# Kernel tuning notes

Measured on AMD Instinct MI355X. Metric: run time of the kernel, lower is better.

## Reference

```python
import jax, jax.numpy as jnp
import numpy as np

SEQ_LEN = 168; PRED_LEN = 24; N_FEAT = 8; KERNEL = 25
N_QUBITS = 4; N_QLAYERS = 2; CONTEXT = 32; HIDDEN = 8; BATCH = 16384
LAG_POSITIONS = [1, 2, 3, 4, 5, 6, 23, 24, 25, 167, 168]
LAG_IDX = np.array([SEQ_LEN - l for l in LAG_POSITIONS if l <= SEQ_LEN])
N_LAGS = int(LAG_IDX.size)
PI = float(np.pi)


def _apply_1q(state, U, w):
    # apply 2x2 gate U (shared (2,2) or per-sample (B,2,2)) on wire w
    state = jnp.moveaxis(state, 1 + w, -1)
    if U.ndim == 2:
        state = jnp.einsum('ij,b...j->b...i', U, state)
    else:
        state = jnp.einsum('bij,b...j->b...i', U, state)
    return jnp.moveaxis(state, -1, 1 + w)


def _apply_cnot(state, c, t):
    ax_c, ax_t = 1 + c, 1 + t
    s0 = jax.lax.index_in_dim(state, 0, ax_c, keepdims=False)
    s1 = jax.lax.index_in_dim(state, 1, ax_c, keepdims=False)
    s1 = jnp.flip(s1, axis=ax_t - (1 if t > c else 0))
    return jnp.stack([s0, s1], axis=ax_c)


def _ry(theta):  # (B,) -> (B,2,2)
    c, s = jnp.cos(theta / 2), jnp.sin(theta / 2)
    return jnp.stack([jnp.stack([c, -s], -1), jnp.stack([s, c], -1)], -2).astype(jnp.complex64)


def _rot(w):  # w (3,): Rot(phi,theta,omega) = RZ(omega) RY(theta) RZ(phi)
    phi, theta, omega = w[0], w[1], w[2]
    c, s = jnp.cos(theta / 2), jnp.sin(theta / 2)
    ep = jnp.exp(-0.5j * (phi + omega))
    em = jnp.exp(0.5j * (phi - omega))
    return jnp.stack([jnp.stack([ep * c, -em * s]),
                      jnp.stack([jnp.conj(em) * s, jnp.conj(ep) * c])]).astype(jnp.complex64)


def _vqc(inputs, weights):
    # data re-uploading: [RY AngleEmbedding -> Rot per wire -> CNOT ring (range 1)] x N_QLAYERS
    # (StronglyEntanglingLayers is called with 1 layer per upload, so range is always 1)
    B = inputs.shape[0]
    state = jnp.zeros((B,) + (2,) * N_QUBITS, jnp.complex64)
    state = state.at[(slice(None),) + (0,) * N_QUBITS].set(1.0)
    for l in range(N_QLAYERS):
        for q in range(N_QUBITS):
            state = _apply_1q(state, _ry(inputs[:, q]), q)
        for q in range(N_QUBITS):
            state = _apply_1q(state, _rot(weights[l, q]), q)
        for q in range(N_QUBITS):
            state = _apply_cnot(state, q, (q + 1) % N_QUBITS)
    probs = state.real ** 2 + state.imag ** 2  # (B,2,2,2,2)
    zdiag = jnp.array([1.0, -1.0], jnp.float32)
    exps = []
    for q in range(N_QUBITS):
        other = tuple(a for a in range(1, N_QUBITS + 1) if a != 1 + q)
        exps.append(jnp.einsum('bq,q->b', probs.sum(other), zdiag))
    return jnp.stack(exps, axis=-1)  # (B, N_QUBITS)


def _decomp(x, decomp_w):
    # learnable moving-average decomposition (DLinear-style, per-feature softmax kernel, edge padding)
    pad = (KERNEL - 1) // 2
    w = jax.nn.softmax(decomp_w, axis=-1)  # (F,K)
    xp = jnp.pad(x, ((0, 0), (pad, KERNEL - 1 - pad), (0, 0)), mode='edge')
    xc = jnp.moveaxis(xp, 1, 2)  # (B,F,S+K-1)
    trend = jax.lax.conv_general_dilated(xc, w[:, None, :], (1,), 'VALID',
                                         feature_group_count=N_FEAT,
                                         dimension_numbers=('NCH', 'OIH', 'NCH'))
    trend = jnp.moveaxis(trend, 1, 2)  # (B,S,F)
    return x - trend, trend


def forward(x, decomp_w, trend_w, trend_b, seasonal_w, seasonal_b, h0_w, h0_b,
            ta_w, ta_b, sc_w, sc_b, crz_w, crz_b, cn_w, cn_b,
            vqc_r, vqc_u, vqc_c, expand_w, expand_b, mod_w, mod_b, fusion_alpha):
    seasonal, trend = _decomp(x, decomp_w)
    trend_out = jnp.einsum('bsf,ps->bpf', trend, trend_w) + trend_b[None, :, None]
    seasonal_base = jnp.einsum('bsf,ps->bpf', seasonal, seasonal_w) + seasonal_b[None, :, None]
    lag_vals = x[:, LAG_IDX, -1]  # (B, N_LAGS), demand is last feature
    h0 = jnp.tanh(lag_vals @ h0_w.T + h0_b)  # (B,H)
    ctx = jnp.einsum('bsf,cs->bfc', seasonal, ta_w) + ta_b  # (B,F,C)
    gru_in = jnp.tanh(ctx.reshape(x.shape[0], -1) @ sc_w.T + sc_b)  # (B,H)
    # single-step quantum GRU
    xh = jnp.concatenate([gru_in, h0], axis=1)  # (B,2H)
    rz_in = jnp.tanh(xh @ crz_w.T + crz_b) * PI  # r_in == z_in (same compress in source)
    r = jax.nn.sigmoid(_vqc(rz_in, vqc_r) @ expand_w.T + expand_b)
    z = jax.nn.sigmoid(_vqc(rz_in, vqc_u) @ expand_w.T + expand_b)
    n_in = jnp.tanh(jnp.concatenate([r * h0, gru_in], axis=1) @ cn_w.T + cn_b) * PI
    n = jnp.tanh(_vqc(n_in, vqc_c) @ expand_w.T + expand_b)
    h_new = (1 - z) * n + z * h0
    modulation = jnp.tanh(h_new @ mod_w.T + mod_b)  # (B,P)
    seasonal_out = seasonal_base * (1.0 + modulation[:, :, None])
    alpha = jax.nn.sigmoid(fusion_alpha)[0]
    return alpha * seasonal_out + (1 - alpha) * trend_out  # (B,P,F)


def setup_inputs() -> dict:
    key = jax.random.key(0)
    ks = iter(jax.random.split(key, 32))

    def lin(out_d, in_d):
        lim = 1.0 / np.sqrt(in_d)
        return (jax.random.uniform(next(ks), (out_d, in_d), jnp.float32, -lim, lim),
                jax.random.uniform(next(ks), (out_d,), jnp.float32, -lim, lim))

    trend_w, trend_b = lin(PRED_LEN, SEQ_LEN)
    seasonal_w, seasonal_b = lin(PRED_LEN, SEQ_LEN)
    h0_w, h0_b = lin(HIDDEN, N_LAGS)
    ta_w, ta_b = lin(CONTEXT, SEQ_LEN)
    sc_w, sc_b = lin(HIDDEN, N_FEAT * CONTEXT)
    crz_w, crz_b = lin(N_QUBITS, 2 * HIDDEN)
    cn_w, cn_b = lin(N_QUBITS, 2 * HIDDEN)
    expand_w, expand_b = lin(HIDDEN, N_QUBITS)
    mod_w, mod_b = lin(PRED_LEN, HIDDEN)
    return {
        'x': jax.random.normal(next(ks), (BATCH, SEQ_LEN, N_FEAT), jnp.float32),
        'decomp_w': 0.02 * jax.random.normal(next(ks), (N_FEAT, KERNEL), jnp.float32),
        'trend_w': trend_w, 'trend_b': trend_b,
        'seasonal_w': seasonal_w, 'seasonal_b': seasonal_b,
        'h0_w': h0_w, 'h0_b': h0_b,
        'ta_w': ta_w, 'ta_b': ta_b,
        'sc_w': sc_w, 'sc_b': sc_b,
        'crz_w': crz_w, 'crz_b': crz_b,
        'cn_w': cn_w, 'cn_b': cn_b,
        'vqc_r': jax.random.uniform(next(ks), (N_QLAYERS, N_QUBITS, 3), jnp.float32, 0.0, 2 * PI),
        'vqc_u': jax.random.uniform(next(ks), (N_QLAYERS, N_QUBITS, 3), jnp.float32, 0.0, 2 * PI),
        'vqc_c': jax.random.uniform(next(ks), (N_QLAYERS, N_QUBITS, 3), jnp.float32, 0.0, 2 * PI),
        'expand_w': expand_w, 'expand_b': expand_b,
        'mod_w': mod_w, 'mod_b': mod_b,
        'fusion_alpha': jnp.array([0.5], jnp.float32),
    }


def reference(x, decomp_w, trend_w, trend_b, seasonal_w, seasonal_b, h0_w, h0_b,
              ta_w, ta_b, sc_w, sc_b, crz_w, crz_b, cn_w, cn_b,
              vqc_r, vqc_u, vqc_c, expand_w, expand_b, mod_w, mod_b, fusion_alpha):
    return forward(x, decomp_w, trend_w, trend_b, seasonal_w, seasonal_b, h0_w, h0_b,
                   ta_w, ta_b, sc_w, sc_b, crz_w, crz_b, cn_w, cn_b,
                   vqc_r, vqc_u, vqc_c, expand_w, expand_b, mod_w, mod_b, fusion_alpha)
```

## Files before the change

### kernel.cpp

```cpp
#include <hip/hip_runtime.h>
#include <hip/hip_bf16.h>
#include <cmath>

#define SEQ   168
#define NF    8
#define PRED  24
#define HID   8
#define KTOT  1344
#define NSCH  6
#define PI_F  3.14159265358979323846f

#define WS_ROTC     256
#define WS_CGIN     512
#define WS_WT       1024
#define WS_IMG_BYTE 524288

typedef __attribute__((ext_vector_type(8))) short bf16x8;
typedef __attribute__((ext_vector_type(4))) float f32x4;

__device__ __forceinline__ float frcp(float x)  { return __builtin_amdgcn_rcpf(x); }
__device__ __forceinline__ float ftanh(float x) {
    float xc = fminf(fmaxf(x, -15.f), 15.f);
    float e  = __expf(2.f * xc);
    return (e - 1.f) * frcp(e + 1.f);
}
__device__ __forceinline__ float sigm(float x) { return frcp(1.f + __expf(-x)); }
__device__ __forceinline__ unsigned short f2bf(float f) {
    __hip_bfloat16 h = __float2bfloat16(f);
    return __builtin_bit_cast(unsigned short, h);
}
__device__ __forceinline__ unsigned pack2(float a, float b) {
    return (unsigned)f2bf(a) | ((unsigned)f2bf(b) << 16);
}

__global__ void k_compose(const float* __restrict__ decomp_w,
                          const float* __restrict__ trend_w,
                          const float* __restrict__ seasonal_w,
                          const float* __restrict__ ta_w,
                          float* __restrict__ Wt) {
    __shared__ float dwsh[NF * 25];
    int t = threadIdx.x;
    if (t < NF) {
        const float* row = decomp_w + t * 25;
        float m = row[0];
        for (int k = 1; k < 25; ++k) m = fmaxf(m, row[k]);
        float e[25]; float sum = 0.f;
        for (int k = 0; k < 25; ++k) { e[k] = expf(row[k] - m); sum += e[k]; }
        float inv = 1.f / sum;
        for (int k = 0; k < 25; ++k) dwsh[t * 25 + k] = e[k] * inv;
    }
    __syncthreads();
    int n = blockIdx.x * 256 + t;
    if (n >= SEQ * 640) return;
    int sx  = n / 640;
    int col = n % 640;
    int j = col >> 3;
    int f = col & 7;
    const float* dwf = dwsh + f * 25;
    const float* wsel;
    int isTrend = 0;
    if (j < 24)      { wsel = trend_w    + j        * SEQ; isTrend = 1; }
    else if (j < 48) { wsel = seasonal_w + (j - 24) * SEQ; }
    else             { wsel = ta_w       + (j - 48) * SEQ; }
    float acc = 0.f;
    if (sx == 0) {
        for (int s = 0; s <= 12; ++s) {
            float cw = 0.f;
            for (int k = 0; k <= 12 - s; ++k) cw += dwf[k];
            acc = fmaf(cw, wsel[s], acc);
        }
    } else if (sx == 167) {
        for (int s = 155; s < 168; ++s) {
            float cw = 0.f;
            for (int k = 179 - s; k < 25; ++k) cw += dwf[k];
            acc = fmaf(cw, wsel[s], acc);
        }
    } else {
        int lo = sx - 12; if (lo < 0) lo = 0;
        int hi = sx + 12; if (hi > 167) hi = 167;
        for (int s = lo; s <= hi; ++s) acc = fmaf(dwf[sx - s + 12], wsel[s], acc);
    }
    Wt[sx * 640 + col] = isTrend ? acc : (wsel[sx] - acc);
}

__global__ void k_img(const float* __restrict__ Wt, const float* __restrict__ sc_w,
                      const float* __restrict__ h0_w,
                      const float* __restrict__ vr, const float* __restrict__ vu,
                      const float* __restrict__ vc,
                      const float* __restrict__ sc_b, const float* __restrict__ ta_b,
                      float* __restrict__ rotc, float* __restrict__ cgin,
                      unsigned char* __restrict__ imgb) {
    int idx = blockIdx.x * 256 + threadIdx.x;
    if (idx < 12288) {
        int lane = idx & 63;
        int rest = idx >> 6;
        int ks = rest % 6;
        int fc = rest / 6;
        int cf = fc & 3, f = fc >> 2;
        int lr = lane & 15, lg = lane >> 4;
        unsigned short vals[8];
        #pragma unroll
        for (int e = 0; e < 8; ++e) {
            int k = ks * 32 + lg * 8 + e;
            float val = 0.f;
            if (k < SEQ) {
                if (cf < 3) {
                    int col = cf * 16 + lr;
                    val = Wt[k * 640 + (col & 1) * 192 + (col >> 1) * 8 + f];
                } else if (lr < 8) {
                    float a = 0.f;
                    for (int cc = 0; cc < 32; ++cc)
                        a = fmaf(sc_w[lr * 256 + f * 32 + cc], Wt[k * 640 + 384 + cc * 8 + f], a);
                    val = a;
                } else if (f == 7) {
                    const int LIDX[11] = {167,166,165,164,163,162,145,144,143,1,0};
                    #pragma unroll
                    for (int i = 0; i < 11; ++i)
                        if (k == LIDX[i]) val = h0_w[(lr - 8) * 11 + i];
                }
            }
            vals[e] = f2bf(val);
        }
        uint4 o;
        o.x = (unsigned)vals[0] | ((unsigned)vals[1] << 16);
        o.y = (unsigned)vals[2] | ((unsigned)vals[3] << 16);
        o.z = (unsigned)vals[4] | ((unsigned)vals[5] << 16);
        o.w = (unsigned)vals[6] | ((unsigned)vals[7] << 16);
        *(uint4*)(imgb + (size_t)rest * 1024 + lane * 16) = o;
    } else if (blockIdx.x == 48) {
        int t = threadIdx.x;
        if (t >= 64 && t < 88) {
            int n = t - 64;
            int v = n / 8, rest = n % 8;
            const float* w = (v == 0 ? vr : (v == 1 ? vu : vc)) + rest * 3;
            float phi = w[0], th = w[1], om = w[2];
            float c = cosf(0.5f * th), s = sinf(0.5f * th);
            float ap = -0.5f * (phi + om);
            float am =  0.5f * (phi - om);
            float* o = rotc + n * 4;
            o[0] = cosf(ap) * c;
            o[1] = sinf(ap) * c;
            o[2] = cosf(am) * s;
            o[3] = sinf(am) * s;
        } else if (t >= 96 && t < 104) {
            int h = t - 96;
            float a = sc_b[h];
            for (int cc = 0; cc < 32; ++cc) {
                float s = 0.f;
                for (int f = 0; f < 8; ++f) s += sc_w[h * 256 + f * 32 + cc];
                a = fmaf(ta_b[cc], s, a);
            }
            cgin[h] = a;
        }
    }
}

__device__ __forceinline__ float shflg(float v, int grp, int idx) {
    return __shfl(v, grp + idx, 64);
}

__device__ void vqc_run(const float cq[4], const float sq[4],
                        const float* __restrict__ rc,
                        int l, int grp, float exps[4]) {
    float re = (l == 0) ? 1.f : 0.f;
    float im = 0.f;
    #pragma unroll
    for (int layer = 0; layer < 2; ++layer) {
        #pragma unroll
        for (int q = 0; q < 4; ++q) {
            int m = 1 << (3 - q);
            float pre = shflg(re, grp, l ^ m);
            float pim = shflg(im, grp, l ^ m);
            float sg = (l & m) ? sq[q] : -sq[q];
            re = cq[q] * re + sg * pre;
            im = cq[q] * im + sg * pim;
        }
        #pragma unroll
        for (int q = 0; q < 4; ++q) {
            int m = 1 << (3 - q);
            const float* g = rc + (layer * 4 + q) * 4;
            float A = g[0], B = g[1], C = g[2], D = g[3];
            float pre = shflg(re, grp, l ^ m);
            float pim = shflg(im, grp, l ^ m);
            float car, cai, cpr, cpi;
            if (l & m) { car = A; cai = -B; cpr =  C; cpi = -D; }
            else       { car = A; cai =  B; cpr = -C; cpi = -D; }
            float nre = car * re - cai * im + cpr * pre - cpi * pim;
            float nim = car * im + cai * re + cpr * pim + cpi * pre;
            re = nre; im = nim;
        }
        #pragma unroll
        for (int q = 0; q < 4; ++q) {
            int mc = 1 << (3 - q);
            int mt = 1 << (3 - ((q + 1) & 3));
            float pre = shflg(re, grp, l ^ mt);
            float pim = shflg(im, grp, l ^ mt);
            if (l & mc) { re = pre; im = pim; }
        }
    }
    float prob = re * re + im * im;
    float v0 = (l & 8) ? -prob : prob;
    float v1 = (l & 4) ? -prob : prob;
    float v2 = (l & 2) ? -prob : prob;
    float v3 = (l & 1) ? -prob : prob;
    #pragma unroll
    for (int m = 1; m < 16; m <<= 1) {
        v0 += __shfl_xor(v0, m, 64);
        v1 += __shfl_xor(v1, m, 64);
        v2 += __shfl_xor(v2, m, 64);
        v3 += __shfl_xor(v3, m, 64);
    }
    exps[0] = v0; exps[1] = v1; exps[2] = v2; exps[3] = v3;
}

__global__ __launch_bounds__(512, 2)
void k_fused(const float* __restrict__ x, const unsigned char* __restrict__ img,
             const float* __restrict__ rotc, const float* __restrict__ cgin,
             const float* __restrict__ h0_b,
             const float* __restrict__ crz_w, const float* __restrict__ crz_b,
             const float* __restrict__ cn_w, const float* __restrict__ cn_b,
             const float* __restrict__ expand_w, const float* __restrict__ expand_b,
             const float* __restrict__ mod_w, const float* __restrict__ mod_b,
             const float* __restrict__ trend_b, const float* __restrict__ seasonal_b,
             const float* __restrict__ fusion_alpha,
             float* __restrict__ out, int Btot)
{
    __shared__ unsigned char lds[114688];
    float* ghpart = (float*)(lds + 98304);
    float* ghbuf  = (float*)lds;
    float* modt   = (float*)(lds + 2304);

    const int t    = threadIdx.x;
    const int b0   = blockIdx.x * 32;
    const int w    = t >> 6, lane = t & 63, lr = lane & 15, lg = lane >> 4;

    const int arow  = t >> 4;
    const int spair = t & 15;
    int gr = b0 + arow; if (gr >= Btot) gr = Btot - 1;
    const float* xrow = x + (size_t)gr * KTOT;

    float4 ra[24];
    #pragma unroll
    for (int kc = 0; kc < NSCH; ++kc) {
        int off = kc * 256 + spair * 16;
        if (off > KTOT - 16) off = KTOT - 16;
        #pragma unroll
        for (int u = 0; u < 4; ++u)
            ra[kc * 4 + u] = *(const float4*)&xrow[off + u * 4];
    }

    bf16x8 Breg[4][NSCH];
    {
        const unsigned char* ib = img + (size_t)(w * 24) * 1024 + (size_t)lane * 16;
        #pragma unroll
        for (int cf = 0; cf < 4; ++cf)
            #pragma unroll
            for (int ks = 0; ks < NSCH; ++ks)
                Breg[cf][ks] = *(const bf16x8*)&ib[(cf * 6 + ks) * 1024];
    }

    #pragma unroll
    for (int kc = 0; kc < NSCH; ++kc) {
        float rfv[16];
        #pragma unroll
        for (int u = 0; u < 4; ++u) {
            rfv[u * 4 + 0] = ra[kc * 4 + u].x; rfv[u * 4 + 1] = ra[kc * 4 + u].y;
            rfv[u * 4 + 2] = ra[kc * 4 + u].z; rfv[u * 4 + 3] = ra[kc * 4 + u].w;
        }
        const int base = kc * 16384;
        const int rb   = (arow * 64 + spair * 4) ^ ((arow & 7) << 4);
        #pragma unroll
        for (int f = 0; f < 8; ++f)
            *(unsigned*)&lds[base + f * 2048 + rb] = pack2(rfv[f], rfv[8 + f]);
    }
    __syncthreads();

    f32x4 acc[3][2], accg[2];
    #pragma unroll
    for (int cf = 0; cf < 3; ++cf) {
        acc[cf][0] = (f32x4){0.f, 0.f, 0.f, 0.f};
        acc[cf][1] = (f32x4){0.f, 0.f, 0.f, 0.f};
    }
    accg[0] = (f32x4){0.f, 0.f, 0.f, 0.f};
    accg[1] = (f32x4){0.f, 0.f, 0.f, 0.f};

    #pragma unroll
    for (int kc = 0; kc < NSCH; ++kc) {
        const int ab = kc * 16384 + w * 2048;
        bf16x8 a0 = *(const bf16x8*)&lds[ab + ((lr * 64 + lg * 16) ^ ((lr & 7) << 4))];
        bf16x8 a1 = *(const bf16x8*)&lds[ab + (((lr + 16) * 64 + lg * 16) ^ ((lr & 7) << 4))];
        #pragma unroll
        for (int cf = 0; cf < 3; ++cf) {
            acc[cf][0] = __builtin_amdgcn_mfma_f32_16x16x32_bf16(a0, Breg[cf][kc], acc[cf][0], 0, 0, 0);
            acc[cf][1] = __builtin_amdgcn_mfma_f32_16x16x32_bf16(a1, Breg[cf][kc], acc[cf][1], 0, 0, 0);
        }
        accg[0] = __builtin_amdgcn_mfma_f32_16x16x32_bf16(a0, Breg[3][kc], accg[0], 0, 0, 0);
        accg[1] = __builtin_amdgcn_mfma_f32_16x16x32_bf16(a1, Breg[3][kc], accg[1], 0, 0, 0);
    }

    #pragma unroll
    for (int mf = 0; mf < 2; ++mf)
        #pragma unroll
        for (int reg = 0; reg < 4; ++reg)
            ghpart[(w * 32 + mf * 16 + lg * 4 + reg) * 16 + lr] = accg[mf][reg];
    __syncthreads();
    {
        int row = t >> 4, col = t & 15;
        float s = 0.f;
        #pragma unroll
        for (int f = 0; f < 8; ++f) s += ghpart[f * 512 + row * 16 + col];
        ghbuf[row * 17 + col] = s;
    }
    __syncthreads();

    {
        const int rl  = t >> 4;
        const int l   = t & 15;
        const int grp = lane & 48;
        float gin[HID], h0v[HID];
        #pragma unroll
        for (int h = 0; h < HID; ++h) {
            gin[h] = ftanh(ghbuf[rl * 17 + h]     + cgin[h]);
            h0v[h] = ftanh(ghbuf[rl * 17 + 8 + h] + h0_b[h]);
        }
        float rz[4];
        #pragma unroll
        for (int q = 0; q < 4; ++q) {
            float a = crz_b[q];
            #pragma unroll
            for (int k = 0; k < 8; ++k) a = fmaf(gin[k], crz_w[q * 16 + k], a);
            #pragma unroll
            for (int k = 0; k < 8; ++k) a = fmaf(h0v[k], crz_w[q * 16 + 8 + k], a);
            rz[q] = ftanh(a) * PI_F;
        }
        float cq[4], sq[4];
        #pragma unroll
        for (int q = 0; q < 4; ++q) { cq[q] = __cosf(0.5f * rz[q]); sq[q] = __sinf(0.5f * rz[q]); }

        float er[4], ez[4];
        vqc_run(cq, sq, rotc + 0 * 32, l, grp, er);
        vqc_run(cq, sq, rotc + 1 * 32, l, grp, ez);

        float rr[HID], zz[HID];
        #pragma unroll
        for (int h = 0; h < HID; ++h) {
            float a = expand_b[h], b = expand_b[h];
            #pragma unroll
            for (int q = 0; q < 4; ++q) {
                a = fmaf(er[q], expand_w[h * 4 + q], a);
                b = fmaf(ez[q], expand_w[h * 4 + q], b);
            }
            rr[h] = sigm(a);
            zz[h] = sigm(b);
        }
        float ni[4];
        #pragma unroll
        for (int q = 0; q < 4; ++q) {
            float a = cn_b[q];
            #pragma unroll
            for (int k = 0; k < 8; ++k) a = fmaf(rr[k] * h0v[k], cn_w[q * 16 + k], a);
            #pragma unroll
            for (int k = 0; k < 8; ++k) a = fmaf(gin[k], cn_w[q * 16 + 8 + k], a);
            ni[q] = ftanh(a) * PI_F;
        }
        #pragma unroll
        for (int q = 0; q < 4; ++q) { cq[q] = __cosf(0.5f * ni[q]); sq[q] = __sinf(0.5f * ni[q]); }
        float en[4];
        vqc_run(cq, sq, rotc + 2 * 32, l, grp, en);

        float hn[HID];
        #pragma unroll
        for (int h = 0; h < HID; ++h) {
            float a = expand_b[h];
            #pragma unroll
            for (int q = 0; q < 4; ++q) a = fmaf(en[q], expand_w[h * 4 + q], a);
            float nn = ftanh(a);
            hn[h] = (1.f - zz[h]) * nn + zz[h] * h0v[h];
        }
        int pp = l;
        float a = mod_b[pp];
        #pragma unroll
        for (int h = 0; h < HID; ++h) a = fmaf(hn[h], mod_w[pp * 8 + h], a);
        modt[rl * 25 + pp] = ftanh(a);
        if (l < 8) {
            pp = l + 16;
            a = mod_b[pp];
            #pragma unroll
            for (int h = 0; h < HID; ++h) a = fmaf(hn[h], mod_w[pp * 8 + h], a);
            modt[rl * 25 + pp] = ftanh(a);
        }
    }
    __syncthreads();

    const float alpha = sigm(fusion_alpha[0]);
    #pragma unroll
    for (int cf = 0; cf < 3; ++cf) {
        int p = cf * 8 + (lr >> 1);
        float tb = trend_b[p], sb = seasonal_b[p];
        #pragma unroll
        for (int mf = 0; mf < 2; ++mf) {
            #pragma unroll
            for (int reg = 0; reg < 4; ++reg) {
                int rl = mf * 16 + lg * 4 + reg;
                float v  = acc[cf][mf][reg];
                float pt = __shfl_xor(v, 1, 64);
                if (!(lr & 1)) {
                    int R = b0 + rl;
                    if (R < Btot) {
                        float md = modt[rl * 25 + p];
                        float res = alpha * ((pt + sb) * (1.f + md))
                                  + (1.f - alpha) * (v + tb);
                        out[(size_t)R * 192 + p * 8 + w] = res;
                    }
                }
            }
        }
    }
}

extern "C" void kernel_launch(void* const* d_in, const int* in_sizes, int n_in,
                              void* d_out, int out_size, void* d_ws, size_t ws_size,
                              hipStream_t stream) {
    const float* x          = (const float*)d_in[0];
    const float* decomp_w   = (const float*)d_in[1];
    const float* trend_w    = (const float*)d_in[2];
    const float* trend_b    = (const float*)d_in[3];
    const float* seasonal_w = (const float*)d_in[4];
    const float* seasonal_b = (const float*)d_in[5];
    const float* h0_w       = (const float*)d_in[6];
    const float* h0_b       = (const float*)d_in[7];
    const float* ta_w       = (const float*)d_in[8];
    const float* ta_b       = (const float*)d_in[9];
    const float* sc_w       = (const float*)d_in[10];
    const float* sc_b       = (const float*)d_in[11];
    const float* crz_w      = (const float*)d_in[12];
    const float* crz_b      = (const float*)d_in[13];
    const float* cn_w       = (const float*)d_in[14];
    const float* cn_b       = (const float*)d_in[15];
    const float* vqc_r      = (const float*)d_in[16];
    const float* vqc_u      = (const float*)d_in[17];
    const float* vqc_c      = (const float*)d_in[18];
    const float* expand_w   = (const float*)d_in[19];
    const float* expand_b   = (const float*)d_in[20];
    const float* mod_w      = (const float*)d_in[21];
    const float* mod_b      = (const float*)d_in[22];
    const float* fus_a      = (const float*)d_in[23];
    float* out = (float*)d_out;

    float* ws   = (float*)d_ws;
    float* rotc = ws + WS_ROTC;
    float* cgin = ws + WS_CGIN;
    float* Wt   = ws + WS_WT;
    unsigned char* img = (unsigned char*)d_ws + WS_IMG_BYTE;

    const int Btot = in_sizes[0] / (SEQ * NF);

    k_compose<<<(SEQ * 640 + 255) / 256, 256, 0, stream>>>(decomp_w, trend_w, seasonal_w, ta_w, Wt);
    k_img<<<49, 256, 0, stream>>>(Wt, sc_w, h0_w, vqc_r, vqc_u, vqc_c, sc_b, ta_b,
                                  rotc, cgin, img);

    k_fused<<<(Btot + 31) / 32, 512, 0, stream>>>(x, img, rotc, cgin, h0_b,
                                                  crz_w, crz_b, cn_w, cn_b,
                                                  expand_w, expand_b, mod_w, mod_b,
                                                  trend_b, seasonal_b, fus_a, out, Btot);
}
```

Baseline: 61.79 us.

## Stream input chunks through a double-buffered LDS ring to raise occupancy

Instead of loading all six K-chunks of x and the B image into registers and staging the whole A tile in LDS up front, the kernel keeps two chunks in flight. Each chunk is written to one of two LDS buffers and consumed by MFMAs, while loads for chunk kc+2 are issued behind it. This cuts the LDS footprint from about 112KB to 48KB and lowers register pressure, and launch bounds are raised to 4 blocks per SM. In exchange it adds a barrier per chunk and exposes more global-load latency inside the loop. The tighter register budget may also cause spills, and with only about 512 blocks the extra occupancy may never be used.

```diff
diff --git a/kernel.cpp b/kernel.cpp
--- a/kernel.cpp
+++ b/kernel.cpp
@@ -213,7 +213,7 @@
     exps[0] = v0; exps[1] = v1; exps[2] = v2; exps[3] = v3;
 }
 
-__global__ __launch_bounds__(512, 2)
+__global__ __launch_bounds__(512, 4)
 void k_fused(const float* __restrict__ x, const unsigned char* __restrict__ img,
              const float* __restrict__ rotc, const float* __restrict__ cgin,
              const float* __restrict__ h0_b,
@@ -225,8 +225,8 @@
              const float* __restrict__ fusion_alpha,
              float* __restrict__ out, int Btot)
 {
-    __shared__ unsigned char lds[114688];
-    float* ghpart = (float*)(lds + 98304);
+    __shared__ unsigned char lds[49152];
+    float* ghpart = (float*)(lds + 32768);
     float* ghbuf  = (float*)lds;
     float* modt   = (float*)(lds + 2304);
 
@@ -239,41 +239,18 @@
     int gr = b0 + arow; if (gr >= Btot) gr = Btot - 1;
     const float* xrow = x + (size_t)gr * KTOT;
 
-    float4 ra[24];
-    #pragma unroll
-    for (int kc = 0; kc < NSCH; ++kc) {
-        int off = kc * 256 + spair * 16;
-        if (off > KTOT - 16) off = KTOT - 16;
-        #pragma unroll
-        for (int u = 0; u < 4; ++u)
-            ra[kc * 4 + u] = *(const float4*)&xrow[off + u * 4];
-    }
-
-    bf16x8 Breg[4][NSCH];
-    {
-        const unsigned char* ib = img + (size_t)(w * 24) * 1024 + (size_t)lane * 16;
-        #pragma unroll
-        for (int cf = 0; cf < 4; ++cf)
-            #pragma unroll
-            for (int ks = 0; ks < NSCH; ++ks)
-                Breg[cf][ks] = *(const bf16x8*)&ib[(cf * 6 + ks) * 1024];
-    }
-
-    #pragma unroll
-    for (int kc = 0; kc < NSCH; ++kc) {
-        float rfv[16];
-        #pragma unroll
-        for (int u = 0; u < 4; ++u) {
-            rfv[u * 4 + 0] = ra[kc * 4 + u].x; rfv[u * 4 + 1] = ra[kc * 4 + u].y;
-            rfv[u * 4 + 2] = ra[kc * 4 + u].z; rfv[u * 4 + 3] = ra[kc * 4 + u].w;
-        }
-        const int base = kc * 16384;
-        const int rb   = (arow * 64 + spair * 4) ^ ((arow & 7) << 4);
-        #pragma unroll
-        for (int f = 0; f < 8; ++f)
-            *(unsigned*)&lds[base + f * 2048 + rb] = pack2(rfv[f], rfv[8 + f]);
-    }
-    __syncthreads();
+    const unsigned char* ib = img + (size_t)(w * 24) * 1024 + (size_t)lane * 16;
+
+    float4 raA[4], raB[4];
+    #pragma unroll
+    for (int u = 0; u < 4; ++u) raA[u] = *(const float4*)&xrow[spair * 16 + u * 4];
+    #pragma unroll
+    for (int u = 0; u < 4; ++u) raB[u] = *(const float4*)&xrow[256 + spair * 16 + u * 4];
+    bf16x8 BrA[4], BrB[4];
+    #pragma unroll
+    for (int cf = 0; cf < 4; ++cf) BrA[cf] = *(const bf16x8*)&ib[(cf * 6 + 0) * 1024];
+    #pragma unroll
+    for (int cf = 0; cf < 4; ++cf) BrB[cf] = *(const bf16x8*)&ib[(cf * 6 + 1) * 1024];
 
     f32x4 acc[3][2], accg[2];
     #pragma unroll
@@ -284,18 +261,61 @@
     accg[0] = (f32x4){0.f, 0.f, 0.f, 0.f};
     accg[1] = (f32x4){0.f, 0.f, 0.f, 0.f};
 
+    const int wb   = (arow * 64 + spair * 4) ^ ((arow & 7) << 4);
+    const int ar0  = (lr * 64 + lg * 16) ^ ((lr & 7) << 4);
+    const int ar1  = ((lr + 16) * 64 + lg * 16) ^ ((lr & 7) << 4);
+
     #pragma unroll
     for (int kc = 0; kc < NSCH; ++kc) {
-        const int ab = kc * 16384 + w * 2048;
-        bf16x8 a0 = *(const bf16x8*)&lds[ab + ((lr * 64 + lg * 16) ^ ((lr & 7) << 4))];
-        bf16x8 a1 = *(const bf16x8*)&lds[ab + (((lr + 16) * 64 + lg * 16) ^ ((lr & 7) << 4))];
-        #pragma unroll
-        for (int cf = 0; cf < 3; ++cf) {
-            acc[cf][0] = __builtin_amdgcn_mfma_f32_16x16x32_bf16(a0, Breg[cf][kc], acc[cf][0], 0, 0, 0);
-            acc[cf][1] = __builtin_amdgcn_mfma_f32_16x16x32_bf16(a1, Breg[cf][kc], acc[cf][1], 0, 0, 0);
-        }
-        accg[0] = __builtin_amdgcn_mfma_f32_16x16x32_bf16(a0, Breg[3][kc], accg[0], 0, 0, 0);
-        accg[1] = __builtin_amdgcn_mfma_f32_16x16x32_bf16(a1, Breg[3][kc], accg[1], 0, 0, 0);
+        const int bufo = (kc & 1) * 16384;
+        {
+            const float* rf = (kc & 1) ? (const float*)raB : (const float*)raA;
+            #pragma unroll
+            for (int f = 0; f < 8; ++f)
+                *(unsigned*)&lds[bufo + f * 2048 + wb] = pack2(rf[f], rf[8 + f]);
+        }
+        if (kc + 2 < NSCH) {
+            int off = (kc + 2) * 256 + spair * 16;
+            if (off > KTOT - 16) off = KTOT - 16;
+            if (kc & 1) {
+                #pragma unroll
+                for (int u = 0; u < 4; ++u) raB[u] = *(const float4*)&xrow[off + u * 4];
+            } else {
+                #pragma unroll
+                for (int u = 0; u < 4; ++u) raA[u] = *(const float4*)&xrow[off + u * 4];
+            }
+        }
+        __syncthreads();
+        {
+            bf16x8 a0 = *(const bf16x8*)&lds[bufo + w * 2048 + ar0];
+            bf16x8 a1 = *(const bf16x8*)&lds[bufo + w * 2048 + ar1];
+            if (kc & 1) {
+                #pragma unroll
+                for (int cf = 0; cf < 3; ++cf) {
+                    acc[cf][0] = __builtin_amdgcn_mfma_f32_16x16x32_bf16(a0, BrB[cf], acc[cf][0], 0, 0, 0);
+                    acc[cf][1] = __builtin_amdgcn_mfma_f32_16x16x32_bf16(a1, BrB[cf], acc[cf][1], 0, 0, 0);
+                }
+                accg[0] = __builtin_amdgcn_mfma_f32_16x16x32_bf16(a0, BrB[3], accg[0], 0, 0, 0);
+                accg[1] = __builtin_amdgcn_mfma_f32_16x16x32_bf16(a1, BrB[3], accg[1], 0, 0, 0);
+            } else {
+                #pragma unroll
+                for (int cf = 0; cf < 3; ++cf) {
+                    acc[cf][0] = __builtin_amdgcn_mfma_f32_16x16x32_bf16(a0, BrA[cf], acc[cf][0], 0, 0, 0);
+                    acc[cf][1] = __builtin_amdgcn_mfma_f32_16x16x32_bf16(a1, BrA[cf], acc[cf][1], 0, 0, 0);
+                }
+                accg[0] = __builtin_amdgcn_mfma_f32_16x16x32_bf16(a0, BrA[3], accg[0], 0, 0, 0);
+                accg[1] = __builtin_amdgcn_mfma_f32_16x16x32_bf16(a1, BrA[3], accg[1], 0, 0, 0);
+            }
+        }
+        if (kc + 2 < NSCH) {
+            if (kc & 1) {
+                #pragma unroll
+                for (int cf = 0; cf < 4; ++cf) BrB[cf] = *(const bf16x8*)&ib[(cf * 6 + kc + 2) * 1024];
+            } else {
+                #pragma unroll
+                for (int cf = 0; cf < 4; ++cf) BrA[cf] = *(const bf16x8*)&ib[(cf * 6 + kc + 2) * 1024];
+            }
+        }
     }
 
     #pragma unroll
```

Measured after the change: 55.06 us. 10.9% less time.

## Stream x chunks through double-buffered LDS to cut shared memory and raise occupancy

Applied to the files above, without the earlier changes.

Before, all six K-chunks of the input tile were staged in LDS at once (about 112KB) and all B fragments were held in registers up front. Now each chunk is packed into one of two 16KB LDS buffers in turn, the next chunk's global load is issued early, and B fragments are loaded per chunk. LDS drops to 32KB and launch bounds ask for 3 blocks per CU, which trades a syncthreads per chunk and less load batching for more resident waves to hide latency. Two buffers with a single barrier per iteration may allow a write to a buffer while another wave still reads it from two chunks earlier.

```diff
diff --git a/kernel.cpp b/kernel.cpp
--- a/kernel.cpp
+++ b/kernel.cpp
@@ -213,7 +213,7 @@
     exps[0] = v0; exps[1] = v1; exps[2] = v2; exps[3] = v3;
 }
 
-__global__ __launch_bounds__(512, 2)
+__global__ __launch_bounds__(512, 3)
 void k_fused(const float* __restrict__ x, const unsigned char* __restrict__ img,
              const float* __restrict__ rotc, const float* __restrict__ cgin,
              const float* __restrict__ h0_b,
@@ -225,10 +225,10 @@
              const float* __restrict__ fusion_alpha,
              float* __restrict__ out, int Btot)
 {
-    __shared__ unsigned char lds[114688];
-    float* ghpart = (float*)(lds + 98304);
-    float* ghbuf  = (float*)lds;
-    float* modt   = (float*)(lds + 2304);
+    __shared__ unsigned char lds[32768];
+    float* ghpart = (float*)lds;
+    float* ghbuf  = (float*)(lds + 16384);
+    float* modt   = (float*)(lds + 16384 + 2304);
 
     const int t    = threadIdx.x;
     const int b0   = blockIdx.x * 32;
@@ -238,42 +238,11 @@
     const int spair = t & 15;
     int gr = b0 + arow; if (gr >= Btot) gr = Btot - 1;
     const float* xrow = x + (size_t)gr * KTOT;
-
-    float4 ra[24];
-    #pragma unroll
-    for (int kc = 0; kc < NSCH; ++kc) {
-        int off = kc * 256 + spair * 16;
-        if (off > KTOT - 16) off = KTOT - 16;
-        #pragma unroll
-        for (int u = 0; u < 4; ++u)
-            ra[kc * 4 + u] = *(const float4*)&xrow[off + u * 4];
-    }
-
-    bf16x8 Breg[4][NSCH];
-    {
-        const unsigned char* ib = img + (size_t)(w * 24) * 1024 + (size_t)lane * 16;
-        #pragma unroll
-        for (int cf = 0; cf < 4; ++cf)
-            #pragma unroll
-            for (int ks = 0; ks < NSCH; ++ks)
-                Breg[cf][ks] = *(const bf16x8*)&ib[(cf * 6 + ks) * 1024];
-    }
-
-    #pragma unroll
-    for (int kc = 0; kc < NSCH; ++kc) {
-        float rfv[16];
-        #pragma unroll
-        for (int u = 0; u < 4; ++u) {
-            rfv[u * 4 + 0] = ra[kc * 4 + u].x; rfv[u * 4 + 1] = ra[kc * 4 + u].y;
-            rfv[u * 4 + 2] = ra[kc * 4 + u].z; rfv[u * 4 + 3] = ra[kc * 4 + u].w;
-        }
-        const int base = kc * 16384;
-        const int rb   = (arow * 64 + spair * 4) ^ ((arow & 7) << 4);
-        #pragma unroll
-        for (int f = 0; f < 8; ++f)
-            *(unsigned*)&lds[base + f * 2048 + rb] = pack2(rfv[f], rfv[8 + f]);
-    }
-    __syncthreads();
+    const unsigned char* ib = img + (size_t)(w * 24) * 1024 + (size_t)lane * 16;
+
+    float4 ra[4];
+    #pragma unroll
+    for (int u = 0; u < 4; ++u) ra[u] = *(const float4*)&xrow[spair * 16 + u * 4];
 
     f32x4 acc[3][2], accg[2];
     #pragma unroll
@@ -284,18 +253,40 @@
     accg[0] = (f32x4){0.f, 0.f, 0.f, 0.f};
     accg[1] = (f32x4){0.f, 0.f, 0.f, 0.f};
 
+    const int wb   = (arow * 64 + spair * 4) ^ ((arow & 7) << 4);
+    const int ar0  = (lr * 64 + lg * 16) ^ ((lr & 7) << 4);
+    const int ar1  = ((lr + 16) * 64 + lg * 16) ^ ((lr & 7) << 4);
+
     #pragma unroll
     for (int kc = 0; kc < NSCH; ++kc) {
-        const int ab = kc * 16384 + w * 2048;
-        bf16x8 a0 = *(const bf16x8*)&lds[ab + ((lr * 64 + lg * 16) ^ ((lr & 7) << 4))];
-        bf16x8 a1 = *(const bf16x8*)&lds[ab + (((lr + 16) * 64 + lg * 16) ^ ((lr & 7) << 4))];
-        #pragma unroll
-        for (int cf = 0; cf < 3; ++cf) {
-            acc[cf][0] = __builtin_amdgcn_mfma_f32_16x16x32_bf16(a0, Breg[cf][kc], acc[cf][0], 0, 0, 0);
-            acc[cf][1] = __builtin_amdgcn_mfma_f32_16x16x32_bf16(a1, Breg[cf][kc], acc[cf][1], 0, 0, 0);
-        }
-        accg[0] = __builtin_amdgcn_mfma_f32_16x16x32_bf16(a0, Breg[3][kc], accg[0], 0, 0, 0);
-        accg[1] = __builtin_amdgcn_mfma_f32_16x16x32_bf16(a1, Breg[3][kc], accg[1], 0, 0, 0);
+        const int bufo = (kc & 1) * 16384;
+        {
+            const float* rf = (const float*)ra;
+            #pragma unroll
+            for (int f = 0; f < 8; ++f)
+                *(unsigned*)&lds[bufo + f * 2048 + wb] = pack2(rf[f], rf[8 + f]);
+        }
+        if (kc + 1 < NSCH) {
+            int off = (kc + 1) * 256 + spair * 16;
+            if (off > KTOT - 16) off = KTOT - 16;
+            #pragma unroll
+            for (int u = 0; u < 4; ++u) ra[u] = *(const float4*)&xrow[off + u * 4];
+        }
+        bf16x8 Br[4];
+        #pragma unroll
+        for (int cf = 0; cf < 4; ++cf) Br[cf] = *(const bf16x8*)&ib[(cf * 6 + kc) * 1024];
+        __syncthreads();
+        {
+            bf16x8 a0 = *(const bf16x8*)&lds[bufo + w * 2048 + ar0];
+            bf16x8 a1 = *(const bf16x8*)&lds[bufo + w * 2048 + ar1];
+            #pragma unroll
+            for (int cf = 0; cf < 3; ++cf) {
+                acc[cf][0] = __builtin_amdgcn_mfma_f32_16x16x32_bf16(a0, Br[cf], acc[cf][0], 0, 0, 0);
+                acc[cf][1] = __builtin_amdgcn_mfma_f32_16x16x32_bf16(a1, Br[cf], acc[cf][1], 0, 0, 0);
+            }
+            accg[0] = __builtin_amdgcn_mfma_f32_16x16x32_bf16(a0, Br[3], accg[0], 0, 0, 0);
+            accg[1] = __builtin_amdgcn_mfma_f32_16x16x32_bf16(a1, Br[3], accg[1], 0, 0, 0);
+        }
     }
 
     #pragma unroll
```

Measured after the change: 49.59 us (median of 3 runs). -19.7%, faster.
